# Performance work log

Hardware: AMD Instinct MI355X
Metric: run time of the kernel (lower is better)

Reference implementation:

```python
import jax, jax.numpy as jnp
import numpy as np

N_WORD = 50000
N_DOC = 10000
E_WW = 800000
E_WD = 320000


def _sage(h_src, h_dst, src, dst, n_dst, W_self, W_neigh, b):
    # DGL SAGEConv('mean'): fc_self(h_dst) + fc_neigh(mean_{u in N(v)} h_u) + bias
    ones = jnp.ones((src.shape[0],), dtype=h_src.dtype)
    deg = jax.ops.segment_sum(ones, dst, num_segments=n_dst)            # [n_dst]
    agg = jax.ops.segment_sum(h_src[src], dst, num_segments=n_dst)      # [n_dst, d]
    mean = agg / jnp.maximum(deg, 1.0)[:, None]                          # zero for isolated
    return h_dst @ W_self + mean @ W_neigh + b


def _layer(xw, xd, edges, Ws, Wn, b):
    (ww_s, ww_d, wwr_s, wwr_d, wd_s, wd_d, wdr_s, wdr_d) = edges
    # relations targeting 'word': word2word, word2wordr, word2documentr
    h_ww = _sage(xw, xw, ww_s, ww_d, N_WORD, Ws[0], Wn[0], b[0])
    h_wwr = _sage(xw, xw, wwr_s, wwr_d, N_WORD, Ws[1], Wn[1], b[1])
    h_wdr = _sage(xd, xw, wdr_s, wdr_d, N_WORD, Ws[3], Wn[3], b[3])
    # relation targeting 'document': word2document
    h_wd = _sage(xw, xd, wd_s, wd_d, N_DOC, Ws[2], Wn[2], b[2])
    # HeteroGraphConv aggregate='stack' then torch.sum(dim=1) == sum over relations; then relu
    return jax.nn.relu(h_ww + h_wwr + h_wdr), jax.nn.relu(h_wd)


def setup_inputs() -> dict:
    key = jax.random.key(0)
    ks = jax.random.split(key, 20)
    d_in, d_h = 256, 128
    inp = {
        "x_word": jax.random.normal(ks[0], (N_WORD, d_in), jnp.float32),
        "x_doc": jax.random.normal(ks[1], (N_DOC, d_in), jnp.float32),
        "ww_src": jax.random.randint(ks[2], (E_WW,), 0, N_WORD, jnp.int32),
        "ww_dst": jax.random.randint(ks[3], (E_WW,), 0, N_WORD, jnp.int32),
        "wwr_src": jax.random.randint(ks[4], (E_WW,), 0, N_WORD, jnp.int32),
        "wwr_dst": jax.random.randint(ks[5], (E_WW,), 0, N_WORD, jnp.int32),
        "wd_src": jax.random.randint(ks[6], (E_WD,), 0, N_WORD, jnp.int32),
        "wd_dst": jax.random.randint(ks[7], (E_WD,), 0, N_DOC, jnp.int32),
        "wdr_src": jax.random.randint(ks[8], (E_WD,), 0, N_DOC, jnp.int32),
        "wdr_dst": jax.random.randint(ks[9], (E_WD,), 0, N_WORD, jnp.int32),
        "Wself1": jax.random.normal(ks[10], (4, d_in, d_h), jnp.float32) * (1.0 / np.sqrt(d_in)),
        "Wneigh1": jax.random.normal(ks[11], (4, d_in, d_h), jnp.float32) * (1.0 / np.sqrt(d_in)),
        "b1": jnp.zeros((4, d_h), jnp.float32),
        "Wself2": jax.random.normal(ks[12], (4, d_h, d_h), jnp.float32) * (1.0 / np.sqrt(d_h)),
        "Wneigh2": jax.random.normal(ks[13], (4, d_h, d_h), jnp.float32) * (1.0 / np.sqrt(d_h)),
        "b2": jnp.zeros((4, d_h), jnp.float32),
        "lin_w": jax.random.normal(ks[14], (1, d_h), jnp.float32) * (1.0 / np.sqrt(d_h)),
        "lin_b": jnp.ones((1,), jnp.float32),
    }
    return inp


def reference(x_word, x_doc, ww_src, ww_dst, wwr_src, wwr_dst, wd_src, wd_dst,
              wdr_src, wdr_dst, Wself1, Wneigh1, b1, Wself2, Wneigh2, b2, lin_w, lin_b):
    edges = (ww_src, ww_dst, wwr_src, wwr_dst, wd_src, wd_dst, wdr_src, wdr_dst)
    xw, xd = _layer(x_word, x_doc, edges, Wself1, Wneigh1, b1)
    xw, xd = _layer(xw, xd, edges, Wself2, Wneigh2, b2)
    out_w = jax.nn.sigmoid(xw @ lin_w.T + lin_b)  # [N_WORD, 1]
    out_d = jax.nn.sigmoid(xd @ lin_w.T + lin_b)  # [N_DOC, 1]
    return out_w, out_d
```

## Files before the change

### kernel.cpp

```cpp
#include <hip/hip_runtime.h>
#include <math.h>

#define N_WORD 50000
#define N_DOC  10000
#define E_WW   800000
#define E_WD   320000
#define D_IN   256
#define D_H    128

#define NPB    256
#define NBK_W  196
#define NBK_D  40
#define BKT    (3 * NBK_W + NBK_D)
#define EPB    4096
#define NBLK_WW 196
#define NBLK_WD 79
#define NBLK_TOT (2 * NBLK_WW + 2 * NBLK_WD)
#define PACK_BLKS 145

#define CAP_WW  4736
#define CAP_WDR 2176
#define CAP_WD  8960

#define WSTRIP ((N_WORD + 63) / 64)
#define DSTRIP ((N_DOC + 63) / 64)
#define NSTRIP (WSTRIP + DSTRIP)

typedef __attribute__((ext_vector_type(8))) short short8;
typedef __attribute__((ext_vector_type(4))) float f32x4;

__device__ inline unsigned short f2bf(float f) {
  unsigned u = __float_as_uint(f);
  u = (u + 0x7fffu + ((u >> 16) & 1u)) >> 16;
  return (unsigned short)u;
}

struct G6 { const short* B[6]; unsigned short* C[6]; };

template <int ABF, int K>
__device__ void gemm_body(const void* __restrict__ Aw, const void* __restrict__ Ad,
                          const G6& g, int blk) {
  constexpr int KT = K >> 5;
  int wid = threadIdx.x >> 6, lane = threadIdx.x & 63;
  const void* A; int M, row0, h0, h1;
  if (blk < WSTRIP) { A = Aw; M = N_WORD; row0 = blk << 6; h0 = 0; h1 = 4; }
  else { A = Ad; M = N_DOC; row0 = (blk - WSTRIP) << 6; h0 = 4; h1 = 6; }
  int r = lane & 15, quad = lane >> 4;
  int m0 = row0 + wid * 16;
  int mA = m0 + r; if (mA >= M) mA = M - 1;
  short8 afr[KT];
  if (ABF) {
    const short* ap = (const short*)A + (size_t)mA * K + quad * 8;
#pragma unroll
    for (int kt = 0; kt < KT; ++kt) afr[kt] = *(const short8*)(ap + kt * 32);
  } else {
    const float* ap = (const float*)A + (size_t)mA * K + quad * 8;
#pragma unroll
    for (int kt = 0; kt < KT; ++kt) {
      float4 a0 = *(const float4*)(ap + kt * 32);
      float4 a1 = *(const float4*)(ap + kt * 32 + 4);
      short8 v;
      v[0] = (short)f2bf(a0.x); v[1] = (short)f2bf(a0.y);
      v[2] = (short)f2bf(a0.z); v[3] = (short)f2bf(a0.w);
      v[4] = (short)f2bf(a1.x); v[5] = (short)f2bf(a1.y);
      v[6] = (short)f2bf(a1.z); v[7] = (short)f2bf(a1.w);
      afr[kt] = v;
    }
  }
  for (int h = h0; h < h1; ++h) {
    const short* Bp = g.B[h];
    f32x4 acc[8];
#pragma unroll
    for (int nt = 0; nt < 8; ++nt) acc[nt] = (f32x4){0.f, 0.f, 0.f, 0.f};
#pragma unroll
    for (int kt = 0; kt < KT; ++kt) {
      const short* bbase = Bp + ((size_t)kt * 4096) + lane * 8;
#pragma unroll
      for (int nt = 0; nt < 8; ++nt) {
        short8 bf = *(const short8*)(bbase + (size_t)nt * 512);
        acc[nt] = __builtin_amdgcn_mfma_f32_16x16x32_bf16(afr[kt], bf, acc[nt], 0, 0, 0);
      }
    }
    unsigned short* C = g.C[h];
#pragma unroll
    for (int nt = 0; nt < 8; ++nt)
#pragma unroll
      for (int rr = 0; rr < 4; ++rr) {
        int row = m0 + quad * 4 + rr;
        if (row < M) C[(size_t)row * 128 + nt * 16 + r] = f2bf(acc[nt][rr]);
      }
  }
}

struct CSRB {
  const unsigned *st_ww, *st_wwr, *st_wdr, *st_wd;
  unsigned short *c_ww, *c_wwr, *c_wdr, *c_wd;
  int *rp_ww, *rp_wwr, *rp_wdr, *rp_wd;
  const int* bcnt;
};

__device__ void place_body(int g, const CSRB& q, int* smem) {
  int* cnt = smem;
  int* off = cnt + 256;
  int* sm  = off + 256;
  const unsigned* st; unsigned short* csr; int* rp; int relFirst, relLast, n, cap, Etot;
  if (g < NBK_W)            { st = q.st_ww;  csr = q.c_ww;  rp = q.rp_ww;  relFirst = 0;         relLast = NBK_W - 1;     n = N_WORD; cap = CAP_WW;  Etot = E_WW; }
  else if (g < 2 * NBK_W)   { st = q.st_wwr; csr = q.c_wwr; rp = q.rp_wwr; relFirst = NBK_W;     relLast = 2 * NBK_W - 1; n = N_WORD; cap = CAP_WW;  Etot = E_WW; }
  else if (g < 3 * NBK_W)   { st = q.st_wdr; csr = q.c_wdr; rp = q.rp_wdr; relFirst = 2 * NBK_W; relLast = 3 * NBK_W - 1; n = N_WORD; cap = CAP_WDR; Etot = E_WD; }
  else                      { st = q.st_wd;  csr = q.c_wd;  rp = q.rp_wd;  relFirst = 3 * NBK_W; relLast = BKT - 1;       n = N_DOC;  cap = CAP_WD;  Etot = E_WD; }
  int cb = g - relFirst;
  int tid = threadIdx.x;
  int v = (tid < cb) ? q.bcnt[relFirst + tid] : 0;
  sm[tid] = v;
  __syncthreads();
  for (int o = 128; o > 0; o >>= 1) {
    if (tid < o) sm[tid] += sm[tid + o];
    __syncthreads();
  }
  int bstart = sm[0];
  if (g == relLast && tid == 0) rp[n] = Etot;
  __syncthreads();
  int node_base = cb << 8;
  int node_cnt = n - node_base; if (node_cnt > NPB) node_cnt = NPB;
  int ecnt = q.bcnt[g];
  const unsigned* w = st + (size_t)cb * cap;
  cnt[tid] = 0;
  __syncthreads();
  for (int j = tid; j < ecnt; j += 256) atomicAdd(&cnt[w[j] >> 16], 1);
  __syncthreads();
  int c = cnt[tid];
  sm[tid] = c;
  __syncthreads();
  for (int o = 1; o < 256; o <<= 1) {
    int add = (tid >= o) ? sm[tid - o] : 0;
    __syncthreads();
    sm[tid] += add;
    __syncthreads();
  }
  int ex = sm[tid] - c;
  off[tid] = ex;
  if (tid < node_cnt) rp[node_base + tid] = bstart + ex;
  __syncthreads();
  for (int j = tid; j < ecnt; j += 256) {
    unsigned e = w[j];
    int p = atomicAdd(&off[e >> 16], 1);
    csr[bstart + p] = (unsigned short)(e & 0xFFFFu);
  }
}

__global__ __launch_bounds__(256, 4) void gemm1_place(
    const float* __restrict__ Aw, const float* __restrict__ Ad, G6 g, CSRB q) {
  __shared__ int smem[768];
  if (blockIdx.x < BKT) place_body(blockIdx.x, q, smem);
  else gemm_body<0, 256>(Aw, Ad, g, blockIdx.x - BKT);
}

__global__ __launch_bounds__(256, 4) void gemm2_kernel(
    const void* __restrict__ Aw, const void* __restrict__ Ad, G6 g) {
  gemm_body<1, 128>(Aw, Ad, g, blockIdx.x);
}

__device__ inline void rel_map(int b, const int* wwd, const int* wwrd, const int* wdrd,
                               const int* wdd, const int*& dst, int& E, int& gbase, int& lb) {
  if (b < NBLK_WW) { dst = wwd; E = E_WW; gbase = 0; lb = b; }
  else if (b < 2 * NBLK_WW) { dst = wwrd; E = E_WW; gbase = NBK_W; lb = b - NBLK_WW; }
  else if (b < 2 * NBLK_WW + NBLK_WD) { dst = wdrd; E = E_WD; gbase = 2 * NBK_W; lb = b - 2 * NBLK_WW; }
  else { dst = wdd; E = E_WD; gbase = 3 * NBK_W; lb = b - 2 * NBLK_WW - NBLK_WD; }
}

__global__ __launch_bounds__(256) void binpack_kernel(
    const int* wws, const int* wwd, const int* wwrs, const int* wwrd,
    const int* wdrs, const int* wdrd, const int* wds, const int* wdd,
    int* bcnt, unsigned* st_ww, unsigned* st_wwr, unsigned* st_wdr, unsigned* st_wd,
    const float* __restrict__ Ws1, const float* __restrict__ Wn1,
    const float* __restrict__ Ws2, const float* __restrict__ Wn2,
    short* __restrict__ Bp1, short* __restrict__ Bp2,
    const float* __restrict__ b1, const float* __restrict__ b2,
    float* __restrict__ bs1, float* __restrict__ bs2) {
  __shared__ int h[4][NBK_W], wb[4][NBK_W], cur[4][NBK_W];
  int b = blockIdx.x;
  if (b >= NBLK_TOT) {
    int tid = (b - NBLK_TOT) * 256 + threadIdx.x;
    const int L1T = 6 * 4096;
    const int L2T = 6 * 2048;
    if (tid >= L1T + L2T) {
      int t = tid - (L1T + L2T);
      if (t < 128) bs1[t] = b1[t] + b1[128 + t] + b1[384 + t];
      else if (t < 256) { int u = t - 128; bs2[u] = b2[u] + b2[128 + u] + b2[384 + u]; }
      return;
    }
    const float *src0, *src1 = nullptr, *src2 = nullptr;
    short* dstp;
    int kt, nt, lane;
    if (tid < L1T) {
      int mat = tid / 4096, rem = tid % 4096;
      kt = rem / 512; nt = (rem / 64) % 8; lane = rem % 64;
      const int W1 = 256 * 128;
      if (mat == 0) { src0 = Ws1; src1 = Ws1 + W1; src2 = Ws1 + 3 * W1; }
      else if (mat <= 4) src0 = Wn1 + (size_t)(mat - 1) * W1;
      else src0 = Ws1 + 2 * W1;
      dstp = Bp1 + (size_t)mat * W1 + ((size_t)(kt * 8 + nt) * 64 + lane) * 8;
    } else {
      int t2 = tid - L1T;
      int mat = t2 / 2048, rem = t2 % 2048;
      kt = rem / 512; nt = (rem / 64) % 8; lane = rem % 64;
      const int W2 = 128 * 128;
      if (mat == 0) { src0 = Ws2; src1 = Ws2 + W2; src2 = Ws2 + 3 * W2; }
      else if (mat <= 4) src0 = Wn2 + (size_t)(mat - 1) * W2;
      else src0 = Ws2 + 2 * W2;
      dstp = Bp2 + (size_t)mat * W2 + ((size_t)(kt * 8 + nt) * 64 + lane) * 8;
    }
    int n = nt * 16 + (lane & 15);
    int kb = kt * 32 + (lane >> 4) * 8;
    short8 v;
#pragma unroll
    for (int j = 0; j < 8; ++j) {
      float f = src0[(size_t)(kb + j) * 128 + n];
      if (src1) f += src1[(size_t)(kb + j) * 128 + n] + src2[(size_t)(kb + j) * 128 + n];
      v[j] = (short)f2bf(f);
    }
    *(short8*)dstp = v;
    return;
  }
  const int* dst; int E, gbase, lb;
  rel_map(b, wwd, wwrd, wdrd, wdd, dst, E, gbase, lb);
  const int* src; unsigned* st; int cap;
  if (b < NBLK_WW) { src = wws; st = st_ww; cap = CAP_WW; }
  else if (b < 2 * NBLK_WW) { src = wwrs; st = st_wwr; cap = CAP_WW; }
  else if (b < 2 * NBLK_WW + NBLK_WD) { src = wdrs; st = st_wdr; cap = CAP_WDR; }
  else { src = wds; st = st_wd; cap = CAP_WD; }
  int tid = threadIdx.x;
  int wave = tid >> 6;
  for (int i = tid; i < 4 * NBK_W; i += 256) { ((int*)h)[i] = 0; ((int*)cur)[i] = 0; }
  __syncthreads();
  int e0 = lb * EPB;
#pragma unroll
  for (int k = 0; k < EPB / 256; ++k) {
    int i = e0 + k * 256 + tid;
    if (i < E) atomicAdd(&h[wave][dst[i] >> 8], 1);
  }
  __syncthreads();
  if (tid < NBK_W) {
    int t0 = h[0][tid], t1 = h[1][tid], t2 = h[2][tid], t3 = h[3][tid];
    int tot = t0 + t1 + t2 + t3;
    int base = tot ? atomicAdd(&bcnt[gbase + tid], tot) : 0;
    wb[0][tid] = base;
    wb[1][tid] = base + t0;
    wb[2][tid] = base + t0 + t1;
    wb[3][tid] = base + t0 + t1 + t2;
  }
  __syncthreads();
#pragma unroll
  for (int k = 0; k < EPB / 256; ++k) {
    int i = e0 + k * 256 + tid;
    if (i < E) {
      int d = dst[i];
      int bk = d >> 8;
      int l = atomicAdd(&cur[wave][bk], 1);
      st[(size_t)bk * cap + wb[wave][bk] + l] =
          (unsigned)(src[i] & 0xFFFF) | ((unsigned)(d & (NPB - 1)) << 16);
    }
  }
}

__device__ inline void accum_rel(const unsigned* __restrict__ y,
                                 const unsigned short* __restrict__ csr,
                                 int beg, int end, int lane, float& f0, float& f1) {
  float a0 = 0.f, a1 = 0.f;
  for (int base = beg; base < end; base += 64) {
    int cnt = end - base; if (cnt > 64) cnt = 64;
    int ld = base + lane; if (ld >= end) ld = end - 1;
    int idx = csr[ld];
    int j = 0;
    for (; j + 7 < cnt; j += 8) {
      unsigned u[8];
#pragma unroll
      for (int k = 0; k < 8; ++k) {
        int s = __builtin_amdgcn_readlane(idx, j + k);
        u[k] = y[((size_t)s << 6) + lane];
      }
#pragma unroll
      for (int k = 0; k < 8; ++k) {
        a0 += __uint_as_float(u[k] << 16);
        a1 += __uint_as_float(u[k] & 0xffff0000u);
      }
    }
    for (; j < cnt; ++j) {
      int s = __builtin_amdgcn_readlane(idx, j);
      unsigned uu = y[((size_t)s << 6) + lane];
      a0 += __uint_as_float(uu << 16);
      a1 += __uint_as_float(uu & 0xffff0000u);
    }
  }
  int deg = end - beg;
  float inv = 1.0f / (float)(deg > 1 ? deg : 1);
  f0 += a0 * inv;
  f1 += a1 * inv;
}

__global__ __launch_bounds__(256) void gather_all(
    const unsigned* __restrict__ y_ww, const unsigned* __restrict__ y_wwr,
    const unsigned* __restrict__ y_wdr, const unsigned* __restrict__ y_wd,
    const unsigned short* __restrict__ c_ww, const unsigned short* __restrict__ c_wwr,
    const unsigned short* __restrict__ c_wdr, const unsigned short* __restrict__ c_wd,
    const int* __restrict__ r_ww, const int* __restrict__ r_wwr,
    const int* __restrict__ r_wdr, const int* __restrict__ r_wd,
    const unsigned* __restrict__ tW, const unsigned* __restrict__ tD,
    const float* __restrict__ bW, const float* __restrict__ bD,
    const float* __restrict__ lw, const float* __restrict__ lb,
    unsigned* __restrict__ oW16, unsigned* __restrict__ oD16,
    float* __restrict__ oF, int mode) {
  int gn = (blockIdx.x << 2) + (threadIdx.x >> 6);
  if (gn >= N_WORD + N_DOC) return;
  int lane = threadIdx.x & 63;
  float f0, f1;
  if (gn < N_WORD) {
    int node = gn;
    unsigned tu = tW[((size_t)node << 6) + lane];
    f0 = __uint_as_float(tu << 16);
    f1 = __uint_as_float(tu & 0xffff0000u);
    accum_rel(y_ww, c_ww, r_ww[node], r_ww[node + 1], lane, f0, f1);
    accum_rel(y_wwr, c_wwr, r_wwr[node], r_wwr[node + 1], lane, f0, f1);
    accum_rel(y_wdr, c_wdr, r_wdr[node], r_wdr[node + 1], lane, f0, f1);
    float2 bv = ((const float2*)bW)[lane];
    f0 = fmaxf(f0 + bv.x, 0.f);
    f1 = fmaxf(f1 + bv.y, 0.f);
    if (mode == 1) {
      oW16[((size_t)node << 6) + lane] = (unsigned)f2bf(f0) | ((unsigned)f2bf(f1) << 16);
    } else {
      float2 lv = ((const float2*)lw)[lane];
      float s = f0 * lv.x + f1 * lv.y;
#pragma unroll
      for (int off = 32; off > 0; off >>= 1) s += __shfl_xor(s, off);
      if (lane == 0) oF[node] = 1.0f / (1.0f + expf(-(s + lb[0])));
    }
  } else {
    int node = gn - N_WORD;
    unsigned tu = tD[((size_t)node << 6) + lane];
    f0 = __uint_as_float(tu << 16);
    f1 = __uint_as_float(tu & 0xffff0000u);
    accum_rel(y_wd, c_wd, r_wd[node], r_wd[node + 1], lane, f0, f1);
    float2 bv = ((const float2*)bD)[lane];
    f0 = fmaxf(f0 + bv.x, 0.f);
    f1 = fmaxf(f1 + bv.y, 0.f);
    if (mode == 1) {
      oD16[((size_t)node << 6) + lane] = (unsigned)f2bf(f0) | ((unsigned)f2bf(f1) << 16);
    } else {
      float2 lv = ((const float2*)lw)[lane];
      float s = f0 * lv.x + f1 * lv.y;
#pragma unroll
      for (int off = 32; off > 0; off >>= 1) s += __shfl_xor(s, off);
      if (lane == 0) oF[N_WORD + node] = 1.0f / (1.0f + expf(-(s + lb[0])));
    }
  }
}

extern "C" void kernel_launch(void* const* d_in, const int* in_sizes, int n_in,
                              void* d_out, int out_size, void* d_ws, size_t ws_size,
                              hipStream_t stream) {
  const float* xw      = (const float*)d_in[0];
  const float* xd      = (const float*)d_in[1];
  const int*   ww_src  = (const int*)d_in[2];
  const int*   ww_dst  = (const int*)d_in[3];
  const int*   wwr_src = (const int*)d_in[4];
  const int*   wwr_dst = (const int*)d_in[5];
  const int*   wd_src  = (const int*)d_in[6];
  const int*   wd_dst  = (const int*)d_in[7];
  const int*   wdr_src = (const int*)d_in[8];
  const int*   wdr_dst = (const int*)d_in[9];
  const float* Ws1     = (const float*)d_in[10];
  const float* Wn1     = (const float*)d_in[11];
  const float* b1      = (const float*)d_in[12];
  const float* Ws2     = (const float*)d_in[13];
  const float* Wn2     = (const float*)d_in[14];
  const float* b2      = (const float*)d_in[15];
  const float* lin_w   = (const float*)d_in[16];
  const float* lin_b   = (const float*)d_in[17];
  float* out = (float*)d_out;

  char* p = (char*)d_ws;
  auto alloc = [&](size_t nbytes) {
    char* r = p;
    p += (nbytes + 255) & ~(size_t)255;
    return r;
  };
  unsigned* twA  = (unsigned*)alloc((size_t)N_WORD * D_H * 2);
  unsigned* tdA  = (unsigned*)alloc((size_t)N_DOC * D_H * 2);
  unsigned* xw1B = (unsigned*)alloc((size_t)N_WORD * D_H * 2);
  unsigned* xd1B = (unsigned*)alloc((size_t)N_DOC * D_H * 2);
  unsigned* yB0 = (unsigned*)alloc((size_t)N_WORD * D_H * 2);
  unsigned* yB1 = (unsigned*)alloc((size_t)N_WORD * D_H * 2);
  unsigned* yB2 = (unsigned*)alloc((size_t)N_WORD * D_H * 2);
  unsigned* ydB = (unsigned*)alloc((size_t)N_DOC * D_H * 2);
  unsigned short* csr_ww  = (unsigned short*)alloc((size_t)E_WW * 2);
  unsigned short* csr_wwr = (unsigned short*)alloc((size_t)E_WW * 2);
  unsigned short* csr_wdr = (unsigned short*)alloc((size_t)E_WD * 2);
  unsigned short* csr_wd  = (unsigned short*)alloc((size_t)E_WD * 2);
  int* rp_ww  = (int*)alloc((size_t)(N_WORD + 1) * 4);
  int* rp_wwr = (int*)alloc((size_t)(N_WORD + 1) * 4);
  int* rp_wdr = (int*)alloc((size_t)(N_WORD + 1) * 4);
  int* rp_wd  = (int*)alloc((size_t)(N_DOC + 1) * 4);
  short* Bp1 = (short*)alloc((size_t)6 * 256 * 128 * 2);
  short* Bp2 = (short*)alloc((size_t)6 * 128 * 128 * 2);
  int* bcnt  = (int*)alloc((size_t)BKT * 4);
  float* bs1 = (float*)alloc(D_H * 4);
  float* bs2 = (float*)alloc(D_H * 4);
  unsigned* yBX = (unsigned*)alloc((size_t)N_WORD * D_H * 2);
  unsigned* st_ww  = yB0;
  unsigned* st_wwr = st_ww + (size_t)NBK_W * CAP_WW;
  unsigned* st_wdr = yB1;
  unsigned* st_wd  = st_wdr + (size_t)NBK_W * CAP_WDR;

  hipMemsetAsync(bcnt, 0, BKT * 4, stream);
  binpack_kernel<<<NBLK_TOT + PACK_BLKS, 256, 0, stream>>>(
      ww_src, ww_dst, wwr_src, wwr_dst, wdr_src, wdr_dst, wd_src, wd_dst,
      bcnt, st_ww, st_wwr, st_wdr, st_wd,
      Ws1, Wn1, Ws2, Wn2, Bp1, Bp2, b1, b2, bs1, bs2);

  const int W1 = 256 * 128;
  const int W2 = 128 * 128;

  G6 g1;
  g1.B[0] = Bp1 + 0 * W1; g1.C[0] = (unsigned short*)twA;
  g1.B[1] = Bp1 + 1 * W1; g1.C[1] = (unsigned short*)yB2;
  g1.B[2] = Bp1 + 2 * W1; g1.C[2] = (unsigned short*)xw1B;
  g1.B[3] = Bp1 + 3 * W1; g1.C[3] = (unsigned short*)yBX;
  g1.B[4] = Bp1 + 5 * W1; g1.C[4] = (unsigned short*)tdA;
  g1.B[5] = Bp1 + 4 * W1; g1.C[5] = (unsigned short*)ydB;
  CSRB q;
  q.st_ww = st_ww; q.st_wwr = st_wwr; q.st_wdr = st_wdr; q.st_wd = st_wd;
  q.c_ww = csr_ww; q.c_wwr = csr_wwr; q.c_wdr = csr_wdr; q.c_wd = csr_wd;
  q.rp_ww = rp_ww; q.rp_wwr = rp_wwr; q.rp_wdr = rp_wdr; q.rp_wd = rp_wd;
  q.bcnt = bcnt;
  gemm1_place<<<BKT + NSTRIP, 256, 0, stream>>>(xw, xd, g1, q);
  gather_all<<<(N_WORD + N_DOC + 3) / 4, 256, 0, stream>>>(
      yB2, xw1B, ydB, yBX, csr_ww, csr_wwr, csr_wdr, csr_wd,
      rp_ww, rp_wwr, rp_wdr, rp_wd, twA, tdA, bs1, b1 + 256,
      lin_w, lin_b, yB0, xd1B, nullptr, 1);

  G6 g2;
  g2.B[0] = Bp2 + 0 * W2; g2.C[0] = (unsigned short*)twA;
  g2.B[1] = Bp2 + 1 * W2; g2.C[1] = (unsigned short*)yB2;
  g2.B[2] = Bp2 + 2 * W2; g2.C[2] = (unsigned short*)xw1B;
  g2.B[3] = Bp2 + 3 * W2; g2.C[3] = (unsigned short*)yBX;
  g2.B[4] = Bp2 + 5 * W2; g2.C[4] = (unsigned short*)tdA;
  g2.B[5] = Bp2 + 4 * W2; g2.C[5] = (unsigned short*)ydB;
  gemm2_kernel<<<NSTRIP, 256, 0, stream>>>(yB0, xd1B, g2);
  gather_all<<<(N_WORD + N_DOC + 3) / 4, 256, 0, stream>>>(
      yB2, xw1B, ydB, yBX, csr_ww, csr_wwr, csr_wdr, csr_wd,
      rp_ww, rp_wwr, rp_wdr, rp_wd, twA, tdA, bs2, b2 + 256,
      lin_w, lin_b, nullptr, nullptr, out, 2);
}
```

Before: 402.9 us.

## Regroup preprocessing: fuse binning with layer-1 GEMM, split placement into own kernel

Weight packing, bias summing and the bucket-count reset move into a small prep kernel that replaces the memset. The edge-binning blocks now run alongside the layer-1 GEMM blocks in one launch, and CSR placement becomes a separate kernel. Binning keeps each thread's destination indices in registers instead of reloading them from global memory. The gemm2 occupancy hint rises to 6. The kernel count stays the same, but which work overlaps with the GEMM changes; the heavier binning work now shares the GEMM launch instead of the lighter placement work.

After: 408.8 us. About the same (+1.5%).

```diff
diff --git a/kernel.cpp b/kernel.cpp
--- a/kernel.cpp
+++ b/kernel.cpp
@@ -92,72 +92,57 @@
   }
 }
 
-struct CSRB {
-  const unsigned *st_ww, *st_wwr, *st_wdr, *st_wd;
-  unsigned short *c_ww, *c_wwr, *c_wdr, *c_wd;
-  int *rp_ww, *rp_wwr, *rp_wdr, *rp_wd;
-  const int* bcnt;
-};
-
-__device__ void place_body(int g, const CSRB& q, int* smem) {
-  int* cnt = smem;
-  int* off = cnt + 256;
-  int* sm  = off + 256;
-  const unsigned* st; unsigned short* csr; int* rp; int relFirst, relLast, n, cap, Etot;
-  if (g < NBK_W)            { st = q.st_ww;  csr = q.c_ww;  rp = q.rp_ww;  relFirst = 0;         relLast = NBK_W - 1;     n = N_WORD; cap = CAP_WW;  Etot = E_WW; }
-  else if (g < 2 * NBK_W)   { st = q.st_wwr; csr = q.c_wwr; rp = q.rp_wwr; relFirst = NBK_W;     relLast = 2 * NBK_W - 1; n = N_WORD; cap = CAP_WW;  Etot = E_WW; }
-  else if (g < 3 * NBK_W)   { st = q.st_wdr; csr = q.c_wdr; rp = q.rp_wdr; relFirst = 2 * NBK_W; relLast = 3 * NBK_W - 1; n = N_WORD; cap = CAP_WDR; Etot = E_WD; }
-  else                      { st = q.st_wd;  csr = q.c_wd;  rp = q.rp_wd;  relFirst = 3 * NBK_W; relLast = BKT - 1;       n = N_DOC;  cap = CAP_WD;  Etot = E_WD; }
-  int cb = g - relFirst;
-  int tid = threadIdx.x;
-  int v = (tid < cb) ? q.bcnt[relFirst + tid] : 0;
-  sm[tid] = v;
-  __syncthreads();
-  for (int o = 128; o > 0; o >>= 1) {
-    if (tid < o) sm[tid] += sm[tid + o];
-    __syncthreads();
-  }
-  int bstart = sm[0];
-  if (g == relLast && tid == 0) rp[n] = Etot;
-  __syncthreads();
-  int node_base = cb << 8;
-  int node_cnt = n - node_base; if (node_cnt > NPB) node_cnt = NPB;
-  int ecnt = q.bcnt[g];
-  const unsigned* w = st + (size_t)cb * cap;
-  cnt[tid] = 0;
-  __syncthreads();
-  for (int j = tid; j < ecnt; j += 256) atomicAdd(&cnt[w[j] >> 16], 1);
-  __syncthreads();
-  int c = cnt[tid];
-  sm[tid] = c;
-  __syncthreads();
-  for (int o = 1; o < 256; o <<= 1) {
-    int add = (tid >= o) ? sm[tid - o] : 0;
-    __syncthreads();
-    sm[tid] += add;
-    __syncthreads();
-  }
-  int ex = sm[tid] - c;
-  off[tid] = ex;
-  if (tid < node_cnt) rp[node_base + tid] = bstart + ex;
-  __syncthreads();
-  for (int j = tid; j < ecnt; j += 256) {
-    unsigned e = w[j];
-    int p = atomicAdd(&off[e >> 16], 1);
-    csr[bstart + p] = (unsigned short)(e & 0xFFFFu);
-  }
-}
-
-__global__ __launch_bounds__(256, 4) void gemm1_place(
-    const float* __restrict__ Aw, const float* __restrict__ Ad, G6 g, CSRB q) {
-  __shared__ int smem[768];
-  if (blockIdx.x < BKT) place_body(blockIdx.x, q, smem);
-  else gemm_body<0, 256>(Aw, Ad, g, blockIdx.x - BKT);
-}
-
-__global__ __launch_bounds__(256, 4) void gemm2_kernel(
-    const void* __restrict__ Aw, const void* __restrict__ Ad, G6 g) {
-  gemm_body<1, 128>(Aw, Ad, g, blockIdx.x);
+__global__ __launch_bounds__(256) void prep_kernel(
+    const float* __restrict__ Ws1, const float* __restrict__ Wn1,
+    const float* __restrict__ Ws2, const float* __restrict__ Wn2,
+    short* __restrict__ Bp1, short* __restrict__ Bp2,
+    const float* __restrict__ b1, const float* __restrict__ b2,
+    float* __restrict__ bs1, float* __restrict__ bs2, int* __restrict__ bcnt) {
+  int b = blockIdx.x;
+  if (b == PACK_BLKS) {
+    for (int i = threadIdx.x; i < BKT; i += 256) bcnt[i] = 0;
+    return;
+  }
+  int tid = b * 256 + threadIdx.x;
+  const int L1T = 6 * 4096;
+  const int L2T = 6 * 2048;
+  if (tid >= L1T + L2T) {
+    int t = tid - (L1T + L2T);
+    if (t < 128) bs1[t] = b1[t] + b1[128 + t] + b1[384 + t];
+    else if (t < 256) { int u = t - 128; bs2[u] = b2[u] + b2[128 + u] + b2[384 + u]; }
+    return;
+  }
+  const float *src0, *src1 = nullptr, *src2 = nullptr;
+  short* dstp;
+  int kt, nt, lane;
+  if (tid < L1T) {
+    int mat = tid / 4096, rem = tid % 4096;
+    kt = rem / 512; nt = (rem / 64) % 8; lane = rem % 64;
+    const int W1 = 256 * 128;
+    if (mat == 0) { src0 = Ws1; src1 = Ws1 + W1; src2 = Ws1 + 3 * W1; }
+    else if (mat <= 4) src0 = Wn1 + (size_t)(mat - 1) * W1;
+    else src0 = Ws1 + 2 * W1;
+    dstp = Bp1 + (size_t)mat * W1 + ((size_t)(kt * 8 + nt) * 64 + lane) * 8;
+  } else {
+    int t2 = tid - L1T;
+    int mat = t2 / 2048, rem = t2 % 2048;
+    kt = rem / 512; nt = (rem / 64) % 8; lane = rem % 64;
+    const int W2 = 128 * 128;
+    if (mat == 0) { src0 = Ws2; src1 = Ws2 + W2; src2 = Ws2 + 3 * W2; }
+    else if (mat <= 4) src0 = Wn2 + (size_t)(mat - 1) * W2;
+    else src0 = Ws2 + 2 * W2;
+    dstp = Bp2 + (size_t)mat * W2 + ((size_t)(kt * 8 + nt) * 64 + lane) * 8;
+  }
+  int n = nt * 16 + (lane & 15);
+  int kb = kt * 32 + (lane >> 4) * 8;
+  short8 v;
+#pragma unroll
+  for (int j = 0; j < 8; ++j) {
+    float f = src0[(size_t)(kb + j) * 128 + n];
+    if (src1) f += src1[(size_t)(kb + j) * 128 + n] + src2[(size_t)(kb + j) * 128 + n];
+    v[j] = (short)f2bf(f);
+  }
+  *(short8*)dstp = v;
 }
 
 __device__ inline void rel_map(int b, const int* wwd, const int* wwrd, const int* wdrd,
@@ -168,58 +153,15 @@
   else { dst = wdd; E = E_WD; gbase = 3 * NBK_W; lb = b - 2 * NBLK_WW - NBLK_WD; }
 }
 
-__global__ __launch_bounds__(256) void binpack_kernel(
+__global__ __launch_bounds__(256, 4) void bin_gemm1(
     const int* wws, const int* wwd, const int* wwrs, const int* wwrd,
     const int* wdrs, const int* wdrd, const int* wds, const int* wdd,
     int* bcnt, unsigned* st_ww, unsigned* st_wwr, unsigned* st_wdr, unsigned* st_wd,
-    const float* __restrict__ Ws1, const float* __restrict__ Wn1,
-    const float* __restrict__ Ws2, const float* __restrict__ Wn2,
-    short* __restrict__ Bp1, short* __restrict__ Bp2,
-    const float* __restrict__ b1, const float* __restrict__ b2,
-    float* __restrict__ bs1, float* __restrict__ bs2) {
+    const float* __restrict__ Aw, const float* __restrict__ Ad, G6 g) {
   __shared__ int h[4][NBK_W], wb[4][NBK_W], cur[4][NBK_W];
   int b = blockIdx.x;
   if (b >= NBLK_TOT) {
-    int tid = (b - NBLK_TOT) * 256 + threadIdx.x;
-    const int L1T = 6 * 4096;
-    const int L2T = 6 * 2048;
-    if (tid >= L1T + L2T) {
-      int t = tid - (L1T + L2T);
-      if (t < 128) bs1[t] = b1[t] + b1[128 + t] + b1[384 + t];
-      else if (t < 256) { int u = t - 128; bs2[u] = b2[u] + b2[128 + u] + b2[384 + u]; }
-      return;
-    }
-    const float *src0, *src1 = nullptr, *src2 = nullptr;
-    short* dstp;
-    int kt, nt, lane;
-    if (tid < L1T) {
-      int mat = tid / 4096, rem = tid % 4096;
-      kt = rem / 512; nt = (rem / 64) % 8; lane = rem % 64;
-      const int W1 = 256 * 128;
-      if (mat == 0) { src0 = Ws1; src1 = Ws1 + W1; src2 = Ws1 + 3 * W1; }
-      else if (mat <= 4) src0 = Wn1 + (size_t)(mat - 1) * W1;
-      else src0 = Ws1 + 2 * W1;
-      dstp = Bp1 + (size_t)mat * W1 + ((size_t)(kt * 8 + nt) * 64 + lane) * 8;
-    } else {
-      int t2 = tid - L1T;
-      int mat = t2 / 2048, rem = t2 % 2048;
-      kt = rem / 512; nt = (rem / 64) % 8; lane = rem % 64;
-      const int W2 = 128 * 128;
-      if (mat == 0) { src0 = Ws2; src1 = Ws2 + W2; src2 = Ws2 + 3 * W2; }
-      else if (mat <= 4) src0 = Wn2 + (size_t)(mat - 1) * W2;
-      else src0 = Ws2 + 2 * W2;
-      dstp = Bp2 + (size_t)mat * W2 + ((size_t)(kt * 8 + nt) * 64 + lane) * 8;
-    }
-    int n = nt * 16 + (lane & 15);
-    int kb = kt * 32 + (lane >> 4) * 8;
-    short8 v;
-#pragma unroll
-    for (int j = 0; j < 8; ++j) {
-      float f = src0[(size_t)(kb + j) * 128 + n];
-      if (src1) f += src1[(size_t)(kb + j) * 128 + n] + src2[(size_t)(kb + j) * 128 + n];
-      v[j] = (short)f2bf(f);
-    }
-    *(short8*)dstp = v;
+    gemm_body<0, 256>(Aw, Ad, g, b - NBLK_TOT);
     return;
   }
   const int* dst; int E, gbase, lb;
@@ -234,10 +176,13 @@
   for (int i = tid; i < 4 * NBK_W; i += 256) { ((int*)h)[i] = 0; ((int*)cur)[i] = 0; }
   __syncthreads();
   int e0 = lb * EPB;
+  int dcache[EPB / 256];
 #pragma unroll
   for (int k = 0; k < EPB / 256; ++k) {
     int i = e0 + k * 256 + tid;
-    if (i < E) atomicAdd(&h[wave][dst[i] >> 8], 1);
+    int d = (i < E) ? dst[i] : -1;
+    dcache[k] = d;
+    if (d >= 0) atomicAdd(&h[wave][d >> 8], 1);
   }
   __syncthreads();
   if (tid < NBK_W) {
@@ -252,15 +197,75 @@
   __syncthreads();
 #pragma unroll
   for (int k = 0; k < EPB / 256; ++k) {
-    int i = e0 + k * 256 + tid;
-    if (i < E) {
-      int d = dst[i];
+    int d = dcache[k];
+    if (d >= 0) {
+      int i = e0 + k * 256 + tid;
       int bk = d >> 8;
       int l = atomicAdd(&cur[wave][bk], 1);
       st[(size_t)bk * cap + wb[wave][bk] + l] =
           (unsigned)(src[i] & 0xFFFF) | ((unsigned)(d & (NPB - 1)) << 16);
     }
   }
+}
+
+struct CSRB {
+  const unsigned *st_ww, *st_wwr, *st_wdr, *st_wd;
+  unsigned short *c_ww, *c_wwr, *c_wdr, *c_wd;
+  int *rp_ww, *rp_wwr, *rp_wdr, *rp_wd;
+  const int* bcnt;
+};
+
+__global__ __launch_bounds__(256) void place_kernel(CSRB q) {
+  __shared__ int cnt[256], off[256], sm[256];
+  int g = blockIdx.x;
+  const unsigned* st; unsigned short* csr; int* rp; int relFirst, relLast, n, cap, Etot;
+  if (g < NBK_W)            { st = q.st_ww;  csr = q.c_ww;  rp = q.rp_ww;  relFirst = 0;         relLast = NBK_W - 1;     n = N_WORD; cap = CAP_WW;  Etot = E_WW; }
+  else if (g < 2 * NBK_W)   { st = q.st_wwr; csr = q.c_wwr; rp = q.rp_wwr; relFirst = NBK_W;     relLast = 2 * NBK_W - 1; n = N_WORD; cap = CAP_WW;  Etot = E_WW; }
+  else if (g < 3 * NBK_W)   { st = q.st_wdr; csr = q.c_wdr; rp = q.rp_wdr; relFirst = 2 * NBK_W; relLast = 3 * NBK_W - 1; n = N_WORD; cap = CAP_WDR; Etot = E_WD; }
+  else                      { st = q.st_wd;  csr = q.c_wd;  rp = q.rp_wd;  relFirst = 3 * NBK_W; relLast = BKT - 1;       n = N_DOC;  cap = CAP_WD;  Etot = E_WD; }
+  int cb = g - relFirst;
+  int tid = threadIdx.x;
+  int v = (tid < cb) ? q.bcnt[relFirst + tid] : 0;
+  sm[tid] = v;
+  __syncthreads();
+  for (int o = 128; o > 0; o >>= 1) {
+    if (tid < o) sm[tid] += sm[tid + o];
+    __syncthreads();
+  }
+  int bstart = sm[0];
+  if (g == relLast && tid == 0) rp[n] = Etot;
+  __syncthreads();
+  int node_base = cb << 8;
+  int node_cnt = n - node_base; if (node_cnt > NPB) node_cnt = NPB;
+  int ecnt = q.bcnt[g];
+  const unsigned* w = st + (size_t)cb * cap;
+  cnt[tid] = 0;
+  __syncthreads();
+  for (int j = tid; j < ecnt; j += 256) atomicAdd(&cnt[w[j] >> 16], 1);
+  __syncthreads();
+  int c = cnt[tid];
+  sm[tid] = c;
+  __syncthreads();
+  for (int o = 1; o < 256; o <<= 1) {
+    int add = (tid >= o) ? sm[tid - o] : 0;
+    __syncthreads();
+    sm[tid] += add;
+    __syncthreads();
+  }
+  int ex = sm[tid] - c;
+  off[tid] = ex;
+  if (tid < node_cnt) rp[node_base + tid] = bstart + ex;
+  __syncthreads();
+  for (int j = tid; j < ecnt; j += 256) {
+    unsigned e = w[j];
+    int p = atomicAdd(&off[e >> 16], 1);
+    csr[bstart + p] = (unsigned short)(e & 0xFFFFu);
+  }
+}
+
+__global__ __launch_bounds__(256, 6) void gemm2_kernel(
+    const void* __restrict__ Aw, const void* __restrict__ Ad, G6 g) {
+  gemm_body<1, 128>(Aw, Ad, g, blockIdx.x);
 }
 
 __device__ inline void accum_rel(const unsigned* __restrict__ y,
@@ -411,14 +416,11 @@
   unsigned* st_wdr = yB1;
   unsigned* st_wd  = st_wdr + (size_t)NBK_W * CAP_WDR;
 
-  hipMemsetAsync(bcnt, 0, BKT * 4, stream);
-  binpack_kernel<<<NBLK_TOT + PACK_BLKS, 256, 0, stream>>>(
-      ww_src, ww_dst, wwr_src, wwr_dst, wdr_src, wdr_dst, wd_src, wd_dst,
-      bcnt, st_ww, st_wwr, st_wdr, st_wd,
-      Ws1, Wn1, Ws2, Wn2, Bp1, Bp2, b1, b2, bs1, bs2);
-
   const int W1 = 256 * 128;
   const int W2 = 128 * 128;
+
+  prep_kernel<<<PACK_BLKS + 1, 256, 0, stream>>>(
+      Ws1, Wn1, Ws2, Wn2, Bp1, Bp2, b1, b2, bs1, bs2, bcnt);
 
   G6 g1;
   g1.B[0] = Bp1 + 0 * W1; g1.C[0] = (unsigned short*)twA;
@@ -427,12 +429,17 @@
   g1.B[3] = Bp1 + 3 * W1; g1.C[3] = (unsigned short*)yBX;
   g1.B[4] = Bp1 + 5 * W1; g1.C[4] = (unsigned short*)tdA;
   g1.B[5] = Bp1 + 4 * W1; g1.C[5] = (unsigned short*)ydB;
+  bin_gemm1<<<NBLK_TOT + NSTRIP, 256, 0, stream>>>(
+      ww_src, ww_dst, wwr_src, wwr_dst, wdr_src, wdr_dst, wd_src, wd_dst,
+      bcnt, st_ww, st_wwr, st_wdr, st_wd, xw, xd, g1);
+
   CSRB q;
   q.st_ww = st_ww; q.st_wwr = st_wwr; q.st_wdr = st_wdr; q.st_wd = st_wd;
   q.c_ww = csr_ww; q.c_wwr = csr_wwr; q.c_wdr = csr_wdr; q.c_wd = csr_wd;
   q.rp_ww = rp_ww; q.rp_wwr = rp_wwr; q.rp_wdr = rp_wdr; q.rp_wd = rp_wd;
   q.bcnt = bcnt;
-  gemm1_place<<<BKT + NSTRIP, 256, 0, stream>>>(xw, xd, g1, q);
+  place_kernel<<<BKT, 256, 0, stream>>>(q);
+
   gather_all<<<(N_WORD + N_DOC + 3) / 4, 256, 0, stream>>>(
       yB2, xw1B, ydB, yBX, csr_ww, csr_wwr, csr_wdr, csr_wd,
       rp_ww, rp_wwr, rp_wdr, rp_wd, twA, tdA, bs1, b1 + 256,
@@ -446,6 +453,7 @@
   g2.B[4] = Bp2 + 5 * W2; g2.C[4] = (unsigned short*)tdA;
   g2.B[5] = Bp2 + 4 * W2; g2.C[5] = (unsigned short*)ydB;
   gemm2_kernel<<<NSTRIP, 256, 0, stream>>>(yB0, xd1B, g2);
+
   gather_all<<<(N_WORD + N_DOC + 3) / 4, 256, 0, stream>>>(
       yB2, xw1B, ydB, yBX, csr_ww, csr_wwr, csr_wdr, csr_wd,
       rp_ww, rp_wwr, rp_wdr, rp_wd, twA, tdA, bs2, b2 + 256,
```
